# Performance work log

Measured on AMD Instinct MI355X. Metric: run time of the kernel, lower is better.

The kernel has to match this reference:

```python
import jax, jax.numpy as jnp
import numpy as np

N = 50000
IN_CH = 128
HEADS = 4
OUT_CH = 16
HID = HEADS * OUT_CH  # 64
E = 800000
B_EXP = 2.0
EPS = 1e-06
LN_EPS = 1e-05

def _l2norm(v, axis):
    n = jnp.sqrt(jnp.sum(v * v, axis=axis, keepdims=True))
    return v / jnp.maximum(n, 1e-12)  # matches F.normalize eps

def setup_inputs() -> dict:
    key = jax.random.key(0)
    k1, k2, k3, k4 = jax.random.split(key, 4)
    x = jax.random.normal(k1, (N, IN_CH), dtype=jnp.float32)
    edge_index = jax.random.randint(k2, (2, E), 0, N, dtype=jnp.int64)
    # lin: xavier_uniform over [HID, IN_CH]
    bound = float(np.sqrt(6.0 / (HID + IN_CH)))
    lin_w = jax.random.uniform(k3, (HID, IN_CH), dtype=jnp.float32, minval=-bound, maxval=bound)
    bcos_w = jax.random.normal(k4, (HID, HID), dtype=jnp.float32) * (1.0 / np.sqrt(HID))
    ln_gamma = jnp.ones((HID,), dtype=jnp.float32)
    ln_beta = jnp.zeros((HID,), dtype=jnp.float32)
    return {"x": x, "edge_index": edge_index, "lin_w": lin_w,
            "bcos_w": bcos_w, "ln_gamma": ln_gamma, "ln_beta": ln_beta}

def reference(x, edge_index, lin_w, bcos_w, ln_gamma, ln_beta):
    row, col = edge_index[0], edge_index[1]
    h = (x @ lin_w.T).reshape(N, HEADS, OUT_CH)          # [N,H,D]
    h_norm = _l2norm(h, axis=2)
    # per-edge cosine between source (col) and target (row) node features
    cos = jnp.sum(h_norm[col] * h_norm[row], axis=2)     # [E,H]
    cos = jnp.clip(cos, EPS, 1.0)
    scale = cos ** (B_EXP - 1.0)                         # [E,H]
    messages = h[col] * scale[:, :, None]                # [E,H,D]
    # scatter-add messages to target nodes
    out = jax.ops.segment_sum(messages.reshape(E, HID), row, num_segments=N)  # [N,HID]
    # BcosLinearNoBias
    lin = out @ bcos_w.T
    o_n = _l2norm(out, axis=1)
    w_n = _l2norm(bcos_w, axis=1)
    cos2 = jnp.clip(o_n @ w_n.T, EPS, 1.0)
    out_bcos = lin * cos2 ** (B_EXP - 1.0)
    # LayerNorm
    mu = jnp.mean(out_bcos, axis=-1, keepdims=True)
    var = jnp.mean((out_bcos - mu) ** 2, axis=-1, keepdims=True)
    out_norm = (out_bcos - mu) / jnp.sqrt(var + LN_EPS) * ln_gamma + ln_beta
    # dropout is identity in eval mode
    return out_norm
```

## Files before the change

kernel.cpp:

```cpp
#include <hip/hip_runtime.h>
#include <math.h>

#define N_NODES 50000
#define IN_CH   128
#define HEADS   4
#define HID     64
#define NEDGE   800000
#define EPS     1e-6f
#define LN_EPS  1e-5f
#define NT4     (N_NODES / 4)
#define PAD     48

#define DPP_ADD_F(p, ctrl) \
    p += __int_as_float(__builtin_amdgcn_update_dpp(0, __float_as_int(p), ctrl, 0xF, 0xF, true))
#define REDUCE16_DPP(p) { DPP_ADD_F(p,0xB1); DPP_ADD_F(p,0x4E); \
                          DPP_ADD_F(p,0x141); DPP_ADD_F(p,0x140); }
#define REDUCE64(p) { REDUCE16_DPP(p); p += __shfl_xor(p,16); p += __shfl_xor(p,32); }

__global__ __launch_bounds__(512) void h_kernel(const float* __restrict__ x,
                                                const float* __restrict__ lin_w,
                                                float* __restrict__ h,
                                                float* __restrict__ inv_hn,
                                                const int* __restrict__ ei,
                                                int* __restrict__ deg,
                                                int* __restrict__ csr_col) {
    __shared__ float4 wt[32 * 65];
    __shared__ float4 xsl[8][128];

    const float4* w4g = (const float4*)lin_w;
    for (int i = threadIdx.x; i < HID * (IN_CH / 4); i += 512) {
        int c = i >> 5, k4 = i & 31;
        wt[k4 * 65 + c] = w4g[i];
    }

    int wave = threadIdx.x >> 6;
    int lane = threadIdx.x & 63;
    int g = blockIdx.x * 8 + wave;
    bool have_g = (g < NT4);

    const float4* xp = (const float4*)x;
    float4 v0, v1;
    if (have_g) {
        v0 = xp[(size_t)g * 128 + lane];
        v1 = xp[(size_t)g * 128 + 64 + lane];
    }

    int t = blockIdx.x * 512 + threadIdx.x;
    bool have_e = (t < NEDGE / 4);
    int4 r, c;
    if (have_e) {
        r = ((const int4*)ei)[t];
        c = ((const int4*)(ei + NEDGE))[t];
    }

    __syncthreads();

    int k0, k1, k2, k3;
    if (have_e) {
        k0 = atomicAdd(&deg[r.x], 1);
        k1 = atomicAdd(&deg[r.y], 1);
        k2 = atomicAdd(&deg[r.z], 1);
        k3 = atomicAdd(&deg[r.w], 1);
    }

    if (have_g) {
        float4* myxs = xsl[wave];
        myxs[lane]      = v0;
        myxs[64 + lane] = v1;

        float a0 = 0.f, a1 = 0.f, a2 = 0.f, a3 = 0.f;
#pragma unroll 2
        for (int k4 = 0; k4 < IN_CH / 4; ++k4) {
            float4 wv = wt[k4 * 65 + lane];
            float4 x0 = myxs[0 * 32 + k4];
            float4 x1 = myxs[1 * 32 + k4];
            float4 x2 = myxs[2 * 32 + k4];
            float4 x3 = myxs[3 * 32 + k4];
            a0 += wv.x * x0.x + wv.y * x0.y + wv.z * x0.z + wv.w * x0.w;
            a1 += wv.x * x1.x + wv.y * x1.y + wv.z * x1.z + wv.w * x1.w;
            a2 += wv.x * x2.x + wv.y * x2.y + wv.z * x2.z + wv.w * x2.w;
            a3 += wv.x * x3.x + wv.y * x3.y + wv.z * x3.z + wv.w * x3.w;
        }

        int n0 = g * 4;
        float accs[4] = {a0, a1, a2, a3};
#pragma unroll
        for (int j = 0; j < 4; ++j) {
            int node = n0 + j;
            h[node * HID + lane] = accs[j];
            float ss = accs[j] * accs[j];
            REDUCE16_DPP(ss);
            if ((lane & 15) == 0)
                inv_hn[node * HEADS + (lane >> 4)] = 1.0f / fmaxf(sqrtf(ss), 1e-12f);
        }
    }

    if (have_e) {
        if (k0 < PAD) __builtin_nontemporal_store(c.x, &csr_col[r.x * PAD + k0]);
        if (k1 < PAD) __builtin_nontemporal_store(c.y, &csr_col[r.y * PAD + k1]);
        if (k2 < PAD) __builtin_nontemporal_store(c.z, &csr_col[r.z * PAD + k2]);
        if (k3 < PAD) __builtin_nontemporal_store(c.w, &csr_col[r.w * PAD + k3]);
    }
}

__global__ __launch_bounds__(256, 4) void gather_final(const int* __restrict__ deg,
                                                       const int* __restrict__ csr_col,
                                                       const float* __restrict__ h,
                                                       const float* __restrict__ inv_hn,
                                                       const float* __restrict__ bcos_w,
                                                       const float* __restrict__ gamma,
                                                       const float* __restrict__ beta,
                                                       float* __restrict__ y) {
    __shared__ float4 wt4[16][65];
    __shared__ float rowbuf[4][HID];
    __shared__ float ivw[HID], gm[HID], bt[HID];

    for (int i = threadIdx.x; i < HID * (HID / 4); i += 256) {
        int j = i >> 4, k4 = i & 15;
        wt4[k4][j] = ((const float4*)bcos_w)[i];
    }
    if (threadIdx.x < HID) {
        gm[threadIdx.x] = gamma[threadIdx.x];
        bt[threadIdx.x] = beta[threadIdx.x];
    }
    __syncthreads();
    if (threadIdx.x < HID) {
        float ss = 0.f;
#pragma unroll
        for (int k4 = 0; k4 < 16; ++k4) {
            float4 q = wt4[k4][threadIdx.x];
            ss += q.x * q.x + q.y * q.y + q.z * q.z + q.w * q.w;
        }
        ivw[threadIdx.x] = 1.0f / fmaxf(sqrtf(ss), 1e-12f);
    }
    __syncthreads();

    int grp  = threadIdx.x >> 6;
    int lane = threadIdx.x & 63;
    int head = lane >> 4;

    for (int g = blockIdx.x; g < N_NODES / 4; g += gridDim.x) {
        int node = g * 4 + grp;
        float hr  = h[node * HID + lane];
        float ihr = inv_hn[node * HEADS + head];
        float hrs = hr * ihr;
        int dg    = __builtin_amdgcn_readfirstlane(min(deg[node], PAD));
        int start = node * PAD;
        int end   = start + dg;

        float ac0 = 0.f, ac1 = 0.f, ac2 = 0.f, ac3 = 0.f;
        int b = start;
#pragma unroll 1
        for (; b + 16 <= end; b += 16) {
            int cc[16];
#pragma unroll
            for (int j = 0; j < 16; ++j) cc[j] = csr_col[b + j];
            float hh[16];
#pragma unroll
            for (int j = 0; j < 16; ++j) hh[j] = h[cc[j] * HID + lane];
            float ii[16];
#pragma unroll
            for (int j = 0; j < 16; ++j) ii[j] = inv_hn[cc[j] * HEADS + head];
#pragma unroll
            for (int j = 0; j < 16; ++j) {
                float p = hh[j] * hrs;
                REDUCE16_DPP(p);
                float s = fminf(fmaxf(p * ii[j], EPS), 1.0f);
                if ((j & 3) == 0)      ac0 = fmaf(hh[j], s, ac0);
                else if ((j & 3) == 1) ac1 = fmaf(hh[j], s, ac1);
                else if ((j & 3) == 2) ac2 = fmaf(hh[j], s, ac2);
                else                   ac3 = fmaf(hh[j], s, ac3);
            }
        }
        int rem = end - b;
        if (rem > 0) {
            int cc[16];
#pragma unroll
            for (int j = 0; j < 16; ++j) cc[j] = csr_col[b + ((j < rem) ? j : rem - 1)];
            float hh[16];
#pragma unroll
            for (int j = 0; j < 16; ++j) hh[j] = h[cc[j] * HID + lane];
            float ii[16];
#pragma unroll
            for (int j = 0; j < 16; ++j) ii[j] = inv_hn[cc[j] * HEADS + head];
#pragma unroll
            for (int j = 0; j < 16; ++j) {
                float p = hh[j] * hrs;
                REDUCE16_DPP(p);
                float s = fminf(fmaxf(p * ii[j], EPS), 1.0f);
                s = (j < rem) ? s : 0.0f;
                if (j & 1) ac1 = fmaf(hh[j], s, ac1);
                else       ac0 = fmaf(hh[j], s, ac0);
            }
        }
        float acc = (ac0 + ac1) + (ac2 + ac3);

        rowbuf[grp][lane] = acc;
        float ss = acc * acc;
        REDUCE64(ss);
        float inv_no = 1.0f / fmaxf(sqrtf(ss), 1e-12f);

        const float4* rb4 = (const float4*)rowbuf[grp];
        float lin = 0.f;
#pragma unroll
        for (int k4 = 0; k4 < 16; ++k4) {
            float4 a  = rb4[k4];
            float4 wv = wt4[k4][lane];
            lin += a.x * wv.x + a.y * wv.y + a.z * wv.z + a.w * wv.w;
        }

        float c2v = lin * inv_no * ivw[lane];
        c2v = fminf(fmaxf(c2v, EPS), 1.0f);
        float ob = lin * c2v;

        float mu = ob;
        REDUCE64(mu);
        mu *= (1.0f / 64.0f);
        float d = ob - mu;
        float var = d * d;
        REDUCE64(var);
        var *= (1.0f / 64.0f);
        float r = rsqrtf(var + LN_EPS);
        y[node * HID + lane] = d * r * gm[lane] + bt[lane];
    }
}

extern "C" void kernel_launch(void* const* d_in, const int* in_sizes, int n_in,
                              void* d_out, int out_size, void* d_ws, size_t ws_size,
                              hipStream_t stream) {
    const float* x      = (const float*)d_in[0];
    const int*   ei     = (const int*)d_in[1];
    const float* lin_w  = (const float*)d_in[2];
    const float* bcos_w = (const float*)d_in[3];
    const float* gamma  = (const float*)d_in[4];
    const float* beta   = (const float*)d_in[5];
    float*       y      = (float*)d_out;

    float* h       = (float*)d_ws;
    float* inv_hn  = h + (size_t)N_NODES * HID;
    int*   deg     = (int*)(inv_hn + (size_t)N_NODES * HEADS);
    int*   csr_col = deg + N_NODES;

    const int H_BLOCKS = (NT4 + 7) / 8;

    hipMemsetAsync(deg, 0, N_NODES * sizeof(int), stream);

    h_kernel<<<H_BLOCKS, 512, 0, stream>>>(x, lin_w, h, inv_hn, ei, deg, csr_col);

    gather_final<<<2048, 256, 0, stream>>>(deg, csr_col, h, inv_hn,
                                           bcos_w, gamma, beta, y);
}
```

Before: 136.9 us.

## Process two nodes per wavefront with interleaved gathers to raise memory parallelism

Each wavefront now handles two destination nodes at once, issuing the neighbor-index and feature gathers for both nodes before doing the reductions. This puts more loads in flight per wave to hide gather latency. The full-chunk and remainder paths are merged into one masked loop, and the epilogue moves into a lambda called once per node. In exchange, register use rises, which may reduce occupancy, and padded lanes do wasted work when the two nodes' degrees differ.

```diff
diff --git a/kernel.cpp b/kernel.cpp
--- a/kernel.cpp
+++ b/kernel.cpp
@@ -139,62 +139,7 @@
     int lane = threadIdx.x & 63;
     int head = lane >> 4;
 
-    for (int g = blockIdx.x; g < N_NODES / 4; g += gridDim.x) {
-        int node = g * 4 + grp;
-        float hr  = h[node * HID + lane];
-        float ihr = inv_hn[node * HEADS + head];
-        float hrs = hr * ihr;
-        int dg    = __builtin_amdgcn_readfirstlane(min(deg[node], PAD));
-        int start = node * PAD;
-        int end   = start + dg;
-
-        float ac0 = 0.f, ac1 = 0.f, ac2 = 0.f, ac3 = 0.f;
-        int b = start;
-#pragma unroll 1
-        for (; b + 16 <= end; b += 16) {
-            int cc[16];
-#pragma unroll
-            for (int j = 0; j < 16; ++j) cc[j] = csr_col[b + j];
-            float hh[16];
-#pragma unroll
-            for (int j = 0; j < 16; ++j) hh[j] = h[cc[j] * HID + lane];
-            float ii[16];
-#pragma unroll
-            for (int j = 0; j < 16; ++j) ii[j] = inv_hn[cc[j] * HEADS + head];
-#pragma unroll
-            for (int j = 0; j < 16; ++j) {
-                float p = hh[j] * hrs;
-                REDUCE16_DPP(p);
-                float s = fminf(fmaxf(p * ii[j], EPS), 1.0f);
-                if ((j & 3) == 0)      ac0 = fmaf(hh[j], s, ac0);
-                else if ((j & 3) == 1) ac1 = fmaf(hh[j], s, ac1);
-                else if ((j & 3) == 2) ac2 = fmaf(hh[j], s, ac2);
-                else                   ac3 = fmaf(hh[j], s, ac3);
-            }
-        }
-        int rem = end - b;
-        if (rem > 0) {
-            int cc[16];
-#pragma unroll
-            for (int j = 0; j < 16; ++j) cc[j] = csr_col[b + ((j < rem) ? j : rem - 1)];
-            float hh[16];
-#pragma unroll
-            for (int j = 0; j < 16; ++j) hh[j] = h[cc[j] * HID + lane];
-            float ii[16];
-#pragma unroll
-            for (int j = 0; j < 16; ++j) ii[j] = inv_hn[cc[j] * HEADS + head];
-#pragma unroll
-            for (int j = 0; j < 16; ++j) {
-                float p = hh[j] * hrs;
-                REDUCE16_DPP(p);
-                float s = fminf(fmaxf(p * ii[j], EPS), 1.0f);
-                s = (j < rem) ? s : 0.0f;
-                if (j & 1) ac1 = fmaf(hh[j], s, ac1);
-                else       ac0 = fmaf(hh[j], s, ac0);
-            }
-        }
-        float acc = (ac0 + ac1) + (ac2 + ac3);
-
+    auto epilogue = [&](int node, float acc) {
         rowbuf[grp][lane] = acc;
         float ss = acc * acc;
         REDUCE64(ss);
@@ -222,6 +167,76 @@
         var *= (1.0f / 64.0f);
         float r = rsqrtf(var + LN_EPS);
         y[node * HID + lane] = d * r * gm[lane] + bt[lane];
+    };
+
+    for (int g = blockIdx.x; g < N_NODES / 8; g += gridDim.x) {
+        int nA = g * 8 + grp * 2;
+        int nB = nA + 1;
+        float hrsA = h[nA * HID + lane] * inv_hn[nA * HEADS + head];
+        float hrsB = h[nB * HID + lane] * inv_hn[nB * HEADS + head];
+        int dgA = __builtin_amdgcn_readfirstlane(min(deg[nA], PAD));
+        int dgB = __builtin_amdgcn_readfirstlane(min(deg[nB], PAD));
+        int baseA = nA * PAD, baseB = nB * PAD;
+        int trips = (max(dgA, dgB) + 15) >> 4;
+
+        float aA0 = 0.f, aA1 = 0.f, aB0 = 0.f, aB1 = 0.f;
+#pragma unroll 1
+        for (int it = 0; it < trips; ++it) {
+            int off = it * 16;
+            bool doA = off < dgA;
+            bool doB = off < dgB;
+
+            int ccA[16], ccB[16];
+            float hhA[16], iiA[16], hhB[16], iiB[16];
+            if (doA) {
+#pragma unroll
+                for (int j = 0; j < 16; ++j) {
+                    int ix = off + j; ix = (ix < dgA) ? ix : dgA - 1;
+                    ccA[j] = csr_col[baseA + ix];
+                }
+#pragma unroll
+                for (int j = 0; j < 16; ++j) hhA[j] = h[ccA[j] * HID + lane];
+#pragma unroll
+                for (int j = 0; j < 16; ++j) iiA[j] = inv_hn[ccA[j] * HEADS + head];
+            }
+            if (doB) {
+#pragma unroll
+                for (int j = 0; j < 16; ++j) {
+                    int ix = off + j; ix = (ix < dgB) ? ix : dgB - 1;
+                    ccB[j] = csr_col[baseB + ix];
+                }
+#pragma unroll
+                for (int j = 0; j < 16; ++j) hhB[j] = h[ccB[j] * HID + lane];
+#pragma unroll
+                for (int j = 0; j < 16; ++j) iiB[j] = inv_hn[ccB[j] * HEADS + head];
+            }
+
+            if (doA) {
+#pragma unroll
+                for (int j = 0; j < 16; ++j) {
+                    float p = hhA[j] * hrsA;
+                    REDUCE16_DPP(p);
+                    float s = fminf(fmaxf(p * iiA[j], EPS), 1.0f);
+                    s = (off + j < dgA) ? s : 0.0f;
+                    if (j & 1) aA1 = fmaf(hhA[j], s, aA1);
+                    else       aA0 = fmaf(hhA[j], s, aA0);
+                }
+            }
+            if (doB) {
+#pragma unroll
+                for (int j = 0; j < 16; ++j) {
+                    float p = hhB[j] * hrsB;
+                    REDUCE16_DPP(p);
+                    float s = fminf(fmaxf(p * iiB[j], EPS), 1.0f);
+                    s = (off + j < dgB) ? s : 0.0f;
+                    if (j & 1) aB1 = fmaf(hhB[j], s, aB1);
+                    else       aB0 = fmaf(hhB[j], s, aB0);
+                }
+            }
+        }
+
+        epilogue(nA, aA0 + aA1);
+        epilogue(nB, aB0 + aB1);
     }
 }
 
```

Result: slower. 339.3 us (+147.9%).

## Process four edges per wavefront with float4 lanes in neighbor aggregation

Applied to the files above, without the earlier changes.

The per-node gather loop is remapped so that each wavefront handles four edges at once: 16 lanes per edge, each lane loading a float4 of the source feature. The per-edge cosine reduction shrinks from a 16-lane DPP chain to a 4-lane one. The four partial accumulators are combined at the end with cross-slot shuffles and written to LDS. This cuts the instruction count per edge and uses wider loads. In exchange it adds masking for partial edge groups and an extra shuffle-and-LDS round trip per node.

```diff
diff --git a/kernel.cpp b/kernel.cpp
--- a/kernel.cpp
+++ b/kernel.cpp
@@ -15,6 +15,7 @@
     p += __int_as_float(__builtin_amdgcn_update_dpp(0, __float_as_int(p), ctrl, 0xF, 0xF, true))
 #define REDUCE16_DPP(p) { DPP_ADD_F(p,0xB1); DPP_ADD_F(p,0x4E); \
                           DPP_ADD_F(p,0x141); DPP_ADD_F(p,0x140); }
+#define REDUCE4_DPP(p)  { DPP_ADD_F(p,0xB1); DPP_ADD_F(p,0x4E); }
 #define REDUCE64(p) { REDUCE16_DPP(p); p += __shfl_xor(p,16); p += __shfl_xor(p,32); }
 
 __global__ __launch_bounds__(512) void h_kernel(const float* __restrict__ x,
@@ -135,68 +136,62 @@
     }
     __syncthreads();
 
-    int grp  = threadIdx.x >> 6;
-    int lane = threadIdx.x & 63;
-    int head = lane >> 4;
+    int grp    = threadIdx.x >> 6;
+    int lane   = threadIdx.x & 63;
+    int e_slot = lane >> 4;
+    int ch4    = lane & 15;
+    int hd     = ch4 >> 2;
+    int head   = lane >> 4;
+
+    const float4* h4 = (const float4*)h;
 
     for (int g = blockIdx.x; g < N_NODES / 4; g += gridDim.x) {
         int node = g * 4 + grp;
-        float hr  = h[node * HID + lane];
-        float ihr = inv_hn[node * HEADS + head];
-        float hrs = hr * ihr;
+        float4 hq  = h4[node * 16 + ch4];
+        float  ihr = inv_hn[node * HEADS + hd];
+        float4 hrs4 = make_float4(hq.x * ihr, hq.y * ihr, hq.z * ihr, hq.w * ihr);
         int dg    = __builtin_amdgcn_readfirstlane(min(deg[node], PAD));
         int start = node * PAD;
-        int end   = start + dg;
-
-        float ac0 = 0.f, ac1 = 0.f, ac2 = 0.f, ac3 = 0.f;
-        int b = start;
+
+        float4 acc = make_float4(0.f, 0.f, 0.f, 0.f);
 #pragma unroll 1
-        for (; b + 16 <= end; b += 16) {
-            int cc[16];
-#pragma unroll
-            for (int j = 0; j < 16; ++j) cc[j] = csr_col[b + j];
-            float hh[16];
-#pragma unroll
-            for (int j = 0; j < 16; ++j) hh[j] = h[cc[j] * HID + lane];
-            float ii[16];
-#pragma unroll
-            for (int j = 0; j < 16; ++j) ii[j] = inv_hn[cc[j] * HEADS + head];
-#pragma unroll
-            for (int j = 0; j < 16; ++j) {
-                float p = hh[j] * hrs;
-                REDUCE16_DPP(p);
-                float s = fminf(fmaxf(p * ii[j], EPS), 1.0f);
-                if ((j & 3) == 0)      ac0 = fmaf(hh[j], s, ac0);
-                else if ((j & 3) == 1) ac1 = fmaf(hh[j], s, ac1);
-                else if ((j & 3) == 2) ac2 = fmaf(hh[j], s, ac2);
-                else                   ac3 = fmaf(hh[j], s, ac3);
+        for (int bb = 0; bb < dg; bb += 16) {
+            int   cc[4];
+            float4 hh[4];
+            float ii[4];
+#pragma unroll
+            for (int s = 0; s < 4; ++s) {
+                int e = bb + s * 4 + e_slot;
+                int ix = (e < dg) ? e : dg - 1;
+                cc[s] = csr_col[start + ix];
             }
-        }
-        int rem = end - b;
-        if (rem > 0) {
-            int cc[16];
-#pragma unroll
-            for (int j = 0; j < 16; ++j) cc[j] = csr_col[b + ((j < rem) ? j : rem - 1)];
-            float hh[16];
-#pragma unroll
-            for (int j = 0; j < 16; ++j) hh[j] = h[cc[j] * HID + lane];
-            float ii[16];
-#pragma unroll
-            for (int j = 0; j < 16; ++j) ii[j] = inv_hn[cc[j] * HEADS + head];
-#pragma unroll
-            for (int j = 0; j < 16; ++j) {
-                float p = hh[j] * hrs;
-                REDUCE16_DPP(p);
-                float s = fminf(fmaxf(p * ii[j], EPS), 1.0f);
-                s = (j < rem) ? s : 0.0f;
-                if (j & 1) ac1 = fmaf(hh[j], s, ac1);
-                else       ac0 = fmaf(hh[j], s, ac0);
+#pragma unroll
+            for (int s = 0; s < 4; ++s) hh[s] = h4[cc[s] * 16 + ch4];
+#pragma unroll
+            for (int s = 0; s < 4; ++s) ii[s] = inv_hn[cc[s] * HEADS + hd];
+#pragma unroll
+            for (int s = 0; s < 4; ++s) {
+                float p = hh[s].x * hrs4.x + hh[s].y * hrs4.y
+                        + hh[s].z * hrs4.z + hh[s].w * hrs4.w;
+                REDUCE4_DPP(p);
+                float sc = fminf(fmaxf(p * ii[s], EPS), 1.0f);
+                int e = bb + s * 4 + e_slot;
+                sc = (e < dg) ? sc : 0.0f;
+                acc.x = fmaf(hh[s].x, sc, acc.x);
+                acc.y = fmaf(hh[s].y, sc, acc.y);
+                acc.z = fmaf(hh[s].z, sc, acc.z);
+                acc.w = fmaf(hh[s].w, sc, acc.w);
             }
         }
-        float acc = (ac0 + ac1) + (ac2 + ac3);
-
-        rowbuf[grp][lane] = acc;
-        float ss = acc * acc;
+        acc.x += __shfl_xor(acc.x, 16); acc.x += __shfl_xor(acc.x, 32);
+        acc.y += __shfl_xor(acc.y, 16); acc.y += __shfl_xor(acc.y, 32);
+        acc.z += __shfl_xor(acc.z, 16); acc.z += __shfl_xor(acc.z, 32);
+        acc.w += __shfl_xor(acc.w, 16); acc.w += __shfl_xor(acc.w, 32);
+
+        if (lane < 16) ((float4*)rowbuf[grp])[ch4] = acc;
+        float o = rowbuf[grp][lane];
+
+        float ss = o * o;
         REDUCE64(ss);
         float inv_no = 1.0f / fmaxf(sqrtf(ss), 1e-12f);
 
@@ -222,6 +217,7 @@
         var *= (1.0f / 64.0f);
         float r = rsqrtf(var + LN_EPS);
         y[node * HID + lane] = d * r * gm[lane] + bt[lane];
+        (void)head;
     }
 }
 
```

Result: faster. 122.1 us (-10.8%).
